# Performance work log

Hardware: AMD Instinct MI355X
Metric: run time of the kernel (lower is better)

## Reference

```python
import jax, jax.numpy as jnp
import numpy as np

BATCH, SEQ, D_IN, D_ST = 16, 8192, 64, 128  # in_features=64, out_features(state)=128


def setup_inputs() -> dict:
    key = jax.random.key(0)
    k0, k1, k2, k3 = jax.random.split(key, 4)
    x = jax.random.normal(k0, (BATCH, SEQ, D_IN), dtype=jnp.float32)
    # State-transition matrix A (HiPPO-initialized in the original). We draw a
    # random dense matrix scaled to spectral radius ~0.9 so the 8192-step
    # recurrence stays numerically stable.
    A = jax.random.normal(k1, (D_ST, D_ST), dtype=jnp.float32) * (0.9 / np.sqrt(D_ST))
    Bw = jax.random.normal(k2, (D_ST, D_IN), dtype=jnp.float32) / np.sqrt(D_IN)
    Bb = jnp.zeros((D_ST,), dtype=jnp.float32)  # bias=True on B
    Cw = jax.random.normal(k3, (D_IN, D_ST), dtype=jnp.float32) / np.sqrt(D_ST)
    return {"x": x, "A": A, "Bw": Bw, "Bb": Bb, "Cw": Cw}


def reference(x, A, Bw, Bb, Cw):
    # Discrete linear SSM: h_t = A h_{t-1} + (B x_t + b),  y_t = C h_t
    # Input projection is batched into one big GEMM (not per-step).
    bx = jnp.einsum('bsi,di->bsd', x, Bw) + Bb          # [B,S,D_ST]
    bx_t = jnp.transpose(bx, (1, 0, 2))                  # [S,B,D_ST]

    def step(h, u):
        h = u + h @ A.T                                  # [B,D_ST]
        return h, h

    h0 = jnp.zeros((x.shape[0], A.shape[0]), dtype=x.dtype)
    _, hs = jax.lax.scan(step, h0, bx_t)                 # hs: [S,B,D_ST]
    # Output projection as one big GEMM after the scan.
    y = jnp.einsum('sbd,od->bso', hs, Cw)                # [B,S,D_IN]
    return y
```

## Files before the change

kernel.cpp:

```cpp
#include <hip/hip_runtime.h>


#define SEQ   8192
#define DIN   64
#define LCH   32
#define NCH   (SEQ / LCH)
#define WFULL 48
#define WTOT  112

typedef _Float16 v8h __attribute__((ext_vector_type(8)));
typedef __fp16   v2h __attribute__((ext_vector_type(2)));
typedef float    v4f __attribute__((ext_vector_type(4)));

#define MFMA(a, b, c) __builtin_amdgcn_mfma_f32_16x16x32_f16((a), (b), (c), 0, 0, 0)
#define PKRTZ __builtin_amdgcn_cvt_pkrtz

__device__ __forceinline__ int rho_inv(int p) {
  int m = p >> 4, q = (p >> 2) & 3, r = p & 3;
  int eh = ((r >> 1) << 1) | (m >> 2);
  int e  = (eh << 1) | (r & 1);
  return 32 * (m & 3) + 8 * q + e;
}

__global__ void prep_kernel(const float* __restrict__ A, const float* __restrict__ Bw,
                            const float* __restrict__ Bb, const float* __restrict__ Cw,
                            _Float16* __restrict__ W, float* __restrict__ Bbs) {
  int idx = blockIdx.x * 256 + threadIdx.x;
  float v; int off_hi, off_lo;
  if (idx < 16384) {
    int p = idx >> 7, j = idx & 127;
    v = A[rho_inv(p) * 128 + j]; off_hi = idx; off_lo = idx + 16384;
  } else if (idx < 24576) {
    int i2 = idx - 16384; int p = i2 >> 6, j = i2 & 63;
    v = Bw[rho_inv(p) * 64 + j]; off_hi = 32768 + i2; off_lo = 40960 + i2;
  } else if (idx < 32768) {
    int i2 = idx - 24576;
    v = Cw[i2]; off_hi = 49152 + i2; off_lo = 57344 + i2;
  } else if (idx < 32896) {
    Bbs[idx - 32768] = Bb[rho_inv(idx - 32768)]; return;
  } else return;
  _Float16 hi = (_Float16)v;
  _Float16 lo = (_Float16)(v - (float)hi);
  W[off_hi] = hi; W[off_lo] = lo;
}

__global__ __launch_bounds__(256, 1) void ssm_kernel(
    const float* __restrict__ x, float* __restrict__ y,
    const _Float16* __restrict__ W, const float* __restrict__ Bbs) {
  const int tid = threadIdx.x;
  const int wv  = tid >> 6;
  const int l   = tid & 63;
  const int n   = l & 15;
  const int q   = l >> 4;
  const int c   = blockIdx.x;
  const int t0  = c * LCH, te = t0 + LCH;
  const int ts  = (t0 > WTOT)  ? (t0 - WTOT)  : 0;
  const int tf  = (t0 > WFULL) ? (t0 - WFULL) : 0;

  const _Float16* Ah = W;
  const _Float16* Al = W + 16384;
  const _Float16* Bh = W + 32768;
  const _Float16* Bl = W + 40960;
  const _Float16* Ch = W + 49152;
  const _Float16* Cl = W + 57344;

  v8h afh[2][4], afl[2][4], bwh[2][2], bwl[2][2], cwh[4], cwl[4];
  v4f bb2[2];
#pragma unroll
  for (int i = 0; i < 2; ++i) {
    int row = 16 * (wv + 4 * i) + n;
#pragma unroll
    for (int kt = 0; kt < 4; ++kt) {
      afh[i][kt] = *(const v8h*)(Ah + row * 128 + 32 * kt + 8 * q);
      afl[i][kt] = *(const v8h*)(Al + row * 128 + 32 * kt + 8 * q);
    }
#pragma unroll
    for (int k2 = 0; k2 < 2; ++k2) {
      bwh[i][k2] = *(const v8h*)(Bh + row * 64 + 32 * k2 + 8 * q);
      bwl[i][k2] = *(const v8h*)(Bl + row * 64 + 32 * k2 + 8 * q);
    }
    bb2[i] = *(const v4f*)(Bbs + 16 * (wv + 4 * i) + 4 * q);
  }
  {
    int row = 16 * wv + n;
#pragma unroll
    for (int kt = 0; kt < 4; ++kt) {
      cwh[kt] = *(const v8h*)(Ch + row * 128 + 32 * kt + 8 * q);
      cwl[kt] = *(const v8h*)(Cl + row * 128 + 32 * kt + 8 * q);
    }
  }

  __shared__ _Float16 hx[2][2][4][512];

  const float* xb = x + (size_t)n * (SEQ * DIN) + 8 * q;
  float* yb = y + (size_t)n * (SEQ * DIN);

  v4f bufA[4], bufB[4];
  auto loadx = [&](v4f(&buf)[4], int t) {
    const float* p = xb + (size_t)t * DIN;
    buf[0] = *(const v4f*)(p);
    buf[1] = *(const v4f*)(p + 4);
    buf[2] = *(const v4f*)(p + 32);
    buf[3] = *(const v4f*)(p + 36);
  };

  v8h hf[4], hlo[4];
#pragma unroll
  for (int kt = 0; kt < 4; ++kt) { hf[kt] = v8h{}; hlo[kt] = v8h{}; }

  v4f uA[2], uB[2];

  auto build_u = [&](const v4f(&b)[4], bool full) {
    union { v2h h2[4]; v8h h8; } H0, H1;
    H0.h2[0] = PKRTZ(b[0][0], b[0][1]); H0.h2[1] = PKRTZ(b[0][2], b[0][3]);
    H0.h2[2] = PKRTZ(b[1][0], b[1][1]); H0.h2[3] = PKRTZ(b[1][2], b[1][3]);
    H1.h2[0] = PKRTZ(b[2][0], b[2][1]); H1.h2[1] = PKRTZ(b[2][2], b[2][3]);
    H1.h2[2] = PKRTZ(b[3][0], b[3][1]); H1.h2[3] = PKRTZ(b[3][2], b[3][3]);
    v8h xh0 = H0.h8, xh1 = H1.h8;
#pragma unroll
    for (int i = 0; i < 2; ++i) {
      v4f a = bb2[i];
      a = MFMA(bwh[i][0], xh0, a);
      a = MFMA(bwh[i][1], xh1, a);
      uA[i] = a;
    }
    if (full) {
      float r[16];
#pragma unroll
      for (int i = 0; i < 8; ++i) r[i]     = b[i >> 2][i & 3]       - (float)H0.h8[i];
#pragma unroll
      for (int i = 0; i < 8; ++i) r[8 + i] = b[2 + (i >> 2)][i & 3] - (float)H1.h8[i];
      union { v2h h2[4]; v8h h8; } L0, L1;
      L0.h2[0] = PKRTZ(r[0], r[1]);   L0.h2[1] = PKRTZ(r[2], r[3]);
      L0.h2[2] = PKRTZ(r[4], r[5]);   L0.h2[3] = PKRTZ(r[6], r[7]);
      L1.h2[0] = PKRTZ(r[8], r[9]);   L1.h2[1] = PKRTZ(r[10], r[11]);
      L1.h2[2] = PKRTZ(r[12], r[13]); L1.h2[3] = PKRTZ(r[14], r[15]);
      v8h xl0 = L0.h8, xl1 = L1.h8;
#pragma unroll
      for (int i = 0; i < 2; ++i) {
        v4f a = {0.f, 0.f, 0.f, 0.f};
        a = MFMA(bwl[i][0], xh0, a);
        a = MFMA(bwl[i][1], xh1, a);
        a = MFMA(bwh[i][0], xl0, a);
        a = MFMA(bwh[i][1], xl1, a);
        uB[i] = a;
      }
    }
  };

  auto emit_y = [&](int t) {
    v4f e1 = {0.f,0.f,0.f,0.f}, e2 = {0.f,0.f,0.f,0.f}, e3 = {0.f,0.f,0.f,0.f};
#pragma unroll
    for (int kt = 0; kt < 4; ++kt) e1 = MFMA(cwh[kt], hf[kt],  e1);
#pragma unroll
    for (int kt = 0; kt < 4; ++kt) e2 = MFMA(cwh[kt], hlo[kt], e2);
#pragma unroll
    for (int kt = 0; kt < 4; ++kt) e3 = MFMA(cwl[kt], hf[kt],  e3);
    v4f r = e1 + e2 + e3;
    *(v4f*)(yb + (size_t)t * DIN + 16 * wv + 4 * q) = r;
  };

  auto xwrite = [&](int pr, const v4f& a0, const v4f& a1, bool full) {
    union { v2h h2[4]; v8h h8; } U;
    U.h2[0] = PKRTZ(a0[0], a0[1]); U.h2[1] = PKRTZ(a1[0], a1[1]);
    U.h2[2] = PKRTZ(a0[2], a0[3]); U.h2[3] = PKRTZ(a1[2], a1[3]);
    *(v8h*)&hx[pr][0][wv][l * 8] = U.h8;
    if (full) {
      float r0 = a0[0] - (float)U.h8[0], r1 = a0[1] - (float)U.h8[1];
      float r2 = a1[0] - (float)U.h8[2], r3 = a1[1] - (float)U.h8[3];
      float r4 = a0[2] - (float)U.h8[4], r5 = a0[3] - (float)U.h8[5];
      float r6 = a1[2] - (float)U.h8[6], r7 = a1[3] - (float)U.h8[7];
      union { v2h h2[4]; v8h h8; } L;
      L.h2[0] = PKRTZ(r0, r1); L.h2[1] = PKRTZ(r2, r3);
      L.h2[2] = PKRTZ(r4, r5); L.h2[3] = PKRTZ(r6, r7);
      *(v8h*)&hx[pr][1][wv][l * 8] = L.h8;
    }
  };

  auto step_full = [&](int t, v4f(&bsrc)[4], v4f(&bld)[4], int pr, bool emit) {
    if (emit) emit_y(t - 1);
    v4f c1[2], c2[2], c3[2];
#pragma unroll
    for (int i = 0; i < 2; ++i) {
      c1[i] = uA[i]; c2[i] = uB[i]; c3[i] = v4f{0.f, 0.f, 0.f, 0.f};
    }
#pragma unroll
    for (int kt = 0; kt < 4; ++kt)
#pragma unroll
      for (int i = 0; i < 2; ++i) {
        c1[i] = MFMA(afh[i][kt], hf[kt],  c1[i]);
        c2[i] = MFMA(afl[i][kt], hf[kt],  c2[i]);
        c3[i] = MFMA(afh[i][kt], hlo[kt], c3[i]);
      }
    build_u(bsrc, true);
    int tn = t + 2; if (tn > SEQ - 1) tn = SEQ - 1;
    loadx(bld, tn);
    v4f a0 = c1[0] + c2[0] + c3[0];
    v4f a1 = c1[1] + c2[1] + c3[1];
    xwrite(pr, a0, a1, true);
    __syncthreads();
#pragma unroll
    for (int kt = 0; kt < 4; ++kt) {
      hf[kt]  = *(const v8h*)&hx[pr][0][kt][l * 8];
      hlo[kt] = *(const v8h*)&hx[pr][1][kt][l * 8];
    }
  };

  auto step_cheap = [&](int t, v4f(&bsrc)[4], v4f(&bld)[4], int pr) {
    v4f c1[2];
#pragma unroll
    for (int i = 0; i < 2; ++i) c1[i] = uA[i];
#pragma unroll
    for (int kt = 0; kt < 4; ++kt)
#pragma unroll
      for (int i = 0; i < 2; ++i) c1[i] = MFMA(afh[i][kt], hf[kt], c1[i]);
    build_u(bsrc, (t + 1) >= tf);
    loadx(bld, t + 2);
    xwrite(pr, c1[0], c1[1], false);
    __syncthreads();
#pragma unroll
    for (int kt = 0; kt < 4; ++kt) hf[kt] = *(const v8h*)&hx[pr][0][kt][l * 8];
  };

  loadx(bufA, ts);
  loadx(bufB, ts + 1);
  build_u(bufA, ts >= tf);

  for (int t = ts; t < tf; t += 2) {
    step_cheap(t,     bufB, bufA, 0);
    step_cheap(t + 1, bufA, bufB, 1);
  }
  for (int t = tf; t < t0; t += 2) {
    step_full(t,     bufB, bufA, 0, false);
    step_full(t + 1, bufA, bufB, 1, false);
  }
  for (int t = t0; t < te; t += 2) {
    step_full(t,     bufB, bufA, 0, t > t0);
    step_full(t + 1, bufA, bufB, 1, true);
  }
  emit_y(te - 1);
}

extern "C" void kernel_launch(void* const* d_in, const int* in_sizes, int n_in,
                              void* d_out, int out_size, void* d_ws, size_t ws_size,
                              hipStream_t stream) {
  const float* x  = (const float*)d_in[0];
  const float* A  = (const float*)d_in[1];
  const float* Bw = (const float*)d_in[2];
  const float* Bb = (const float*)d_in[3];
  const float* Cw = (const float*)d_in[4];
  float* y = (float*)d_out;

  _Float16* W   = (_Float16*)d_ws;
  float*    Bbs = (float*)(W + 65536);

  prep_kernel<<<129, 256, 0, stream>>>(A, Bw, Bb, Cw, W, Bbs);
  ssm_kernel<<<NCH, 256, 0, stream>>>(x, y, W, Bbs);
}
```

Measured before the change: 102.3 us.

## Replace warmup-window recurrence with two-pass chunked scan using precomputed powers of A

Drops the per-chunk 112-step warmup recomputation. A first pass computes each 16-step chunk's local final state, and a second pass combines the previous up to 7 chunk states with precomputed powers of A (A^16 through A^96, built by small matmul kernels) to form each chunk's initial state. It then reruns the chunk to emit y. MFMA accumulation chains are also split into independent partial sums to shorten dependency latency. The cost is nine extra small kernel launches, two passes over x, and a truncated combine that depends on A's spectral decay.

Result: slower. 135.9 us (+32.8%).

```diff
diff --git a/kernel.cpp b/kernel.cpp
--- a/kernel.cpp
+++ b/kernel.cpp
@@ -3,10 +3,9 @@
 
 #define SEQ   8192
 #define DIN   64
-#define LCH   32
+#define LCH   16
 #define NCH   (SEQ / LCH)
-#define WFULL 48
-#define WTOT  112
+#define KCOMB 7
 
 typedef _Float16 v8h __attribute__((ext_vector_type(8)));
 typedef __fp16   v2h __attribute__((ext_vector_type(2)));
@@ -14,39 +13,93 @@
 
 #define MFMA(a, b, c) __builtin_amdgcn_mfma_f32_16x16x32_f16((a), (b), (c), 0, 0, 0)
 #define PKRTZ __builtin_amdgcn_cvt_pkrtz
-
+#define Z4 (v4f{0.f, 0.f, 0.f, 0.f})
+
+
+__device__ __forceinline__ int rho_fwd(int lidx) {
+  int kt = lidx >> 5, q = (lidx >> 3) & 3, e = lidx & 7;
+  int eh = e >> 1;
+  int m = kt + 4 * (eh & 1);
+  int r = 2 * (eh >> 1) + (e & 1);
+  return 16 * m + 4 * q + r;
+}
 __device__ __forceinline__ int rho_inv(int p) {
   int m = p >> 4, q = (p >> 2) & 3, r = p & 3;
   int eh = ((r >> 1) << 1) | (m >> 2);
   int e  = (eh << 1) | (r & 1);
   return 32 * (m & 3) + 8 * q + e;
 }
-
-__global__ void prep_kernel(const float* __restrict__ A, const float* __restrict__ Bw,
-                            const float* __restrict__ Bb, const float* __restrict__ Cw,
-                            _Float16* __restrict__ W, float* __restrict__ Bbs) {
+__device__ __forceinline__ void pack_hl(float v, _Float16* hp, _Float16* lp) {
+  _Float16 h = (_Float16)v;
+  *hp = h; *lp = (_Float16)(v - (float)h);
+}
+
+__global__ void mmk(const float* x0, const float* y0, float* d0,
+                    const float* x1, const float* y1, float* d1,
+                    const float* x2, const float* y2, float* d2) {
+  int which = blockIdx.x >> 6;
+  const float* X = (which == 0) ? x0 : ((which == 1) ? x1 : x2);
+  const float* Y = (which == 0) ? y0 : ((which == 1) ? y1 : y2);
+  float*       D = (which == 0) ? d0 : ((which == 1) ? d1 : d2);
+  int idx = (blockIdx.x & 63) * 256 + threadIdx.x;
+  int i = idx >> 7, j = idx & 127;
+  float s = 0.f;
+  for (int k = 0; k < 128; ++k) s = fmaf(X[i * 128 + k], Y[k * 128 + j], s);
+  D[idx] = s;
+}
+
+__global__ void packk(const float* __restrict__ A, const float* __restrict__ Bw,
+                      const float* __restrict__ Bb, const float* __restrict__ Cw,
+                      const float* __restrict__ pw, _Float16* __restrict__ F,
+                      float* __restrict__ Bbs) {
   int idx = blockIdx.x * 256 + threadIdx.x;
-  float v; int off_hi, off_lo;
   if (idx < 16384) {
-    int p = idx >> 7, j = idx & 127;
-    v = A[rho_inv(p) * 128 + j]; off_hi = idx; off_lo = idx + 16384;
+    int i = idx >> 7, j = idx & 127;
+    int o = rho_fwd(i) * 128 + j;
+    pack_hl(A[idx], F + o, F + 16384 + o);
   } else if (idx < 24576) {
-    int i2 = idx - 16384; int p = i2 >> 6, j = i2 & 63;
-    v = Bw[rho_inv(p) * 64 + j]; off_hi = 32768 + i2; off_lo = 40960 + i2;
+    int p = idx - 16384; int i = p >> 6, j = p & 63;
+    int o = rho_fwd(i) * 64 + j;
+    pack_hl(Bw[p], F + 32768 + o, F + 40960 + o);
   } else if (idx < 32768) {
-    int i2 = idx - 24576;
-    v = Cw[i2]; off_hi = 49152 + i2; off_lo = 57344 + i2;
+    int p = idx - 24576;
+    pack_hl(Cw[p], F + 49152 + p, F + 57344 + p);
   } else if (idx < 32896) {
-    Bbs[idx - 32768] = Bb[rho_inv(idx - 32768)]; return;
-  } else return;
-  _Float16 hi = (_Float16)v;
-  _Float16 lo = (_Float16)(v - (float)hi);
-  W[off_hi] = hi; W[off_lo] = lo;
-}
-
-__global__ __launch_bounds__(256, 1) void ssm_kernel(
-    const float* __restrict__ x, float* __restrict__ y,
-    const _Float16* __restrict__ W, const float* __restrict__ Bbs) {
+    int i = idx - 32768;
+    Bbs[i] = Bb[rho_inv(i)];
+  } else if (idx < 147584) {
+    int p = idx - 32896;
+    int k = p >> 14, r = p & 16383;
+    int i = r >> 7, j = r & 127;
+    float v = (k == 0) ? ((i == j) ? 1.f : 0.f) : pw[(k + 2) * 16384 + r];
+    int o = rho_fwd(i) * 128 + j;
+    pack_hl(v, F + 65536 + k * 16384 + o, F + 180224 + k * 16384 + o);
+  }
+}
+
+__device__ __forceinline__ void split16(const v4f* b, v8h& xh0, v8h& xh1,
+                                        v8h& xl0, v8h& xl1) {
+  union { v2h h2[4]; v8h h8; } H0, H1;
+  H0.h2[0] = PKRTZ(b[0][0], b[0][1]); H0.h2[1] = PKRTZ(b[0][2], b[0][3]);
+  H0.h2[2] = PKRTZ(b[1][0], b[1][1]); H0.h2[3] = PKRTZ(b[1][2], b[1][3]);
+  H1.h2[0] = PKRTZ(b[2][0], b[2][1]); H1.h2[1] = PKRTZ(b[2][2], b[2][3]);
+  H1.h2[2] = PKRTZ(b[3][0], b[3][1]); H1.h2[3] = PKRTZ(b[3][2], b[3][3]);
+  float r[16];
+#pragma unroll
+  for (int i = 0; i < 8; ++i) r[i]     = b[i >> 2][i & 3]       - (float)H0.h8[i];
+#pragma unroll
+  for (int i = 0; i < 8; ++i) r[8 + i] = b[2 + (i >> 2)][i & 3] - (float)H1.h8[i];
+  union { v2h h2[4]; v8h h8; } L0, L1;
+  L0.h2[0] = PKRTZ(r[0], r[1]);   L0.h2[1] = PKRTZ(r[2], r[3]);
+  L0.h2[2] = PKRTZ(r[4], r[5]);   L0.h2[3] = PKRTZ(r[6], r[7]);
+  L1.h2[0] = PKRTZ(r[8], r[9]);   L1.h2[1] = PKRTZ(r[10], r[11]);
+  L1.h2[2] = PKRTZ(r[12], r[13]); L1.h2[3] = PKRTZ(r[14], r[15]);
+  xh0 = H0.h8; xh1 = H1.h8; xl0 = L0.h8; xl1 = L1.h8;
+}
+
+__global__ __launch_bounds__(256, 2) void scan1(
+    const float* __restrict__ x, const _Float16* __restrict__ F,
+    const float* __restrict__ Bbs, _Float16* __restrict__ Vbuf) {
   const int tid = threadIdx.x;
   const int wv  = tid >> 6;
   const int l   = tid & 63;
@@ -54,17 +107,13 @@
   const int q   = l >> 4;
   const int c   = blockIdx.x;
   const int t0  = c * LCH, te = t0 + LCH;
-  const int ts  = (t0 > WTOT)  ? (t0 - WTOT)  : 0;
-  const int tf  = (t0 > WFULL) ? (t0 - WFULL) : 0;
-
-  const _Float16* Ah = W;
-  const _Float16* Al = W + 16384;
-  const _Float16* Bh = W + 32768;
-  const _Float16* Bl = W + 40960;
-  const _Float16* Ch = W + 49152;
-  const _Float16* Cl = W + 57344;
-
-  v8h afh[2][4], afl[2][4], bwh[2][2], bwl[2][2], cwh[4], cwl[4];
+
+  const _Float16* Ah = F;
+  const _Float16* Al = F + 16384;
+  const _Float16* Bh = F + 32768;
+  const _Float16* Bl = F + 40960;
+
+  v8h afh[2][4], afl[2][4], bwh[2][2], bwl[2][2];
   v4f bb2[2];
 #pragma unroll
   for (int i = 0; i < 2; ++i) {
@@ -81,123 +130,255 @@
     }
     bb2[i] = *(const v4f*)(Bbs + 16 * (wv + 4 * i) + 4 * q);
   }
-  {
-    int row = 16 * wv + n;
-#pragma unroll
-    for (int kt = 0; kt < 4; ++kt) {
-      cwh[kt] = *(const v8h*)(Ch + row * 128 + 32 * kt + 8 * q);
-      cwl[kt] = *(const v8h*)(Cl + row * 128 + 32 * kt + 8 * q);
-    }
-  }
 
   __shared__ _Float16 hx[2][2][4][512];
 
   const float* xb = x + (size_t)n * (SEQ * DIN) + 8 * q;
-  float* yb = y + (size_t)n * (SEQ * DIN);
-
-  v4f bufA[4], bufB[4];
+  v4f bufA[4], bufB[4], uA[2], uB[2];
   auto loadx = [&](v4f(&buf)[4], int t) {
     const float* p = xb + (size_t)t * DIN;
-    buf[0] = *(const v4f*)(p);
-    buf[1] = *(const v4f*)(p + 4);
-    buf[2] = *(const v4f*)(p + 32);
-    buf[3] = *(const v4f*)(p + 36);
-  };
-
-  v8h hf[4], hlo[4];
-#pragma unroll
-  for (int kt = 0; kt < 4; ++kt) { hf[kt] = v8h{}; hlo[kt] = v8h{}; }
-
-  v4f uA[2], uB[2];
-
-  auto build_u = [&](const v4f(&b)[4], bool full) {
-    union { v2h h2[4]; v8h h8; } H0, H1;
-    H0.h2[0] = PKRTZ(b[0][0], b[0][1]); H0.h2[1] = PKRTZ(b[0][2], b[0][3]);
-    H0.h2[2] = PKRTZ(b[1][0], b[1][1]); H0.h2[3] = PKRTZ(b[1][2], b[1][3]);
-    H1.h2[0] = PKRTZ(b[2][0], b[2][1]); H1.h2[1] = PKRTZ(b[2][2], b[2][3]);
-    H1.h2[2] = PKRTZ(b[3][0], b[3][1]); H1.h2[3] = PKRTZ(b[3][2], b[3][3]);
-    v8h xh0 = H0.h8, xh1 = H1.h8;
+    buf[0] = *(const v4f*)(p);     buf[1] = *(const v4f*)(p + 4);
+    buf[2] = *(const v4f*)(p + 32); buf[3] = *(const v4f*)(p + 36);
+  };
+  auto build_u = [&](const v4f(&b)[4]) {
+    v8h xh0, xh1, xl0, xl1;
+    split16(b, xh0, xh1, xl0, xl1);
 #pragma unroll
     for (int i = 0; i < 2; ++i) {
       v4f a = bb2[i];
       a = MFMA(bwh[i][0], xh0, a);
       a = MFMA(bwh[i][1], xh1, a);
       uA[i] = a;
-    }
-    if (full) {
-      float r[16];
-#pragma unroll
-      for (int i = 0; i < 8; ++i) r[i]     = b[i >> 2][i & 3]       - (float)H0.h8[i];
-#pragma unroll
-      for (int i = 0; i < 8; ++i) r[8 + i] = b[2 + (i >> 2)][i & 3] - (float)H1.h8[i];
-      union { v2h h2[4]; v8h h8; } L0, L1;
-      L0.h2[0] = PKRTZ(r[0], r[1]);   L0.h2[1] = PKRTZ(r[2], r[3]);
-      L0.h2[2] = PKRTZ(r[4], r[5]);   L0.h2[3] = PKRTZ(r[6], r[7]);
-      L1.h2[0] = PKRTZ(r[8], r[9]);   L1.h2[1] = PKRTZ(r[10], r[11]);
-      L1.h2[2] = PKRTZ(r[12], r[13]); L1.h2[3] = PKRTZ(r[14], r[15]);
-      v8h xl0 = L0.h8, xl1 = L1.h8;
-#pragma unroll
-      for (int i = 0; i < 2; ++i) {
-        v4f a = {0.f, 0.f, 0.f, 0.f};
-        a = MFMA(bwl[i][0], xh0, a);
-        a = MFMA(bwl[i][1], xh1, a);
-        a = MFMA(bwh[i][0], xl0, a);
-        a = MFMA(bwh[i][1], xl1, a);
-        uB[i] = a;
-      }
-    }
-  };
-
-  auto emit_y = [&](int t) {
-    v4f e1 = {0.f,0.f,0.f,0.f}, e2 = {0.f,0.f,0.f,0.f}, e3 = {0.f,0.f,0.f,0.f};
-#pragma unroll
-    for (int kt = 0; kt < 4; ++kt) e1 = MFMA(cwh[kt], hf[kt],  e1);
-#pragma unroll
-    for (int kt = 0; kt < 4; ++kt) e2 = MFMA(cwh[kt], hlo[kt], e2);
-#pragma unroll
-    for (int kt = 0; kt < 4; ++kt) e3 = MFMA(cwl[kt], hf[kt],  e3);
-    v4f r = e1 + e2 + e3;
-    *(v4f*)(yb + (size_t)t * DIN + 16 * wv + 4 * q) = r;
-  };
-
-  auto xwrite = [&](int pr, const v4f& a0, const v4f& a1, bool full) {
+      v4f b1 = MFMA(bwl[i][0], xh0, Z4);
+      b1 = MFMA(bwl[i][1], xh1, b1);
+      v4f b2 = MFMA(bwh[i][0], xl0, Z4);
+      b2 = MFMA(bwh[i][1], xl1, b2);
+      uB[i] = b1 + b2;
+    }
+  };
+  auto xwrite = [&](int pr, const v4f& a0, const v4f& a1) {
     union { v2h h2[4]; v8h h8; } U;
     U.h2[0] = PKRTZ(a0[0], a0[1]); U.h2[1] = PKRTZ(a1[0], a1[1]);
     U.h2[2] = PKRTZ(a0[2], a0[3]); U.h2[3] = PKRTZ(a1[2], a1[3]);
     *(v8h*)&hx[pr][0][wv][l * 8] = U.h8;
-    if (full) {
-      float r0 = a0[0] - (float)U.h8[0], r1 = a0[1] - (float)U.h8[1];
-      float r2 = a1[0] - (float)U.h8[2], r3 = a1[1] - (float)U.h8[3];
-      float r4 = a0[2] - (float)U.h8[4], r5 = a0[3] - (float)U.h8[5];
-      float r6 = a1[2] - (float)U.h8[6], r7 = a1[3] - (float)U.h8[7];
-      union { v2h h2[4]; v8h h8; } L;
-      L.h2[0] = PKRTZ(r0, r1); L.h2[1] = PKRTZ(r2, r3);
-      L.h2[2] = PKRTZ(r4, r5); L.h2[3] = PKRTZ(r6, r7);
-      *(v8h*)&hx[pr][1][wv][l * 8] = L.h8;
-    }
-  };
-
+    float r0 = a0[0] - (float)U.h8[0], r1 = a0[1] - (float)U.h8[1];
+    float r2 = a1[0] - (float)U.h8[2], r3 = a1[1] - (float)U.h8[3];
+    float r4 = a0[2] - (float)U.h8[4], r5 = a0[3] - (float)U.h8[5];
+    float r6 = a1[2] - (float)U.h8[6], r7 = a1[3] - (float)U.h8[7];
+    union { v2h h2[4]; v8h h8; } L;
+    L.h2[0] = PKRTZ(r0, r1); L.h2[1] = PKRTZ(r2, r3);
+    L.h2[2] = PKRTZ(r4, r5); L.h2[3] = PKRTZ(r6, r7);
+    *(v8h*)&hx[pr][1][wv][l * 8] = L.h8;
+  };
+
+  v8h hf[4], hlo[4];
+#pragma unroll
+  for (int kt = 0; kt < 4; ++kt) { hf[kt] = v8h{}; hlo[kt] = v8h{}; }
+
+  auto step_full = [&](int t, v4f(&bsrc)[4], v4f(&bld)[4], int pr) {
+    v4f acc[2];
+#pragma unroll
+    for (int i = 0; i < 2; ++i) {
+      v4f a = MFMA(afh[i][0], hf[0], uA[i]);
+      a     = MFMA(afh[i][1], hf[1], a);
+      v4f b = MFMA(afh[i][2], hf[2], Z4);
+      b     = MFMA(afh[i][3], hf[3], b);
+      v4f c2a = MFMA(afl[i][0], hf[0], uB[i]);
+      c2a     = MFMA(afl[i][1], hf[1], c2a);
+      v4f c2b = MFMA(afl[i][2], hf[2], Z4);
+      c2b     = MFMA(afl[i][3], hf[3], c2b);
+      v4f c3a = MFMA(afh[i][0], hlo[0], Z4);
+      c3a     = MFMA(afh[i][1], hlo[1], c3a);
+      v4f c3b = MFMA(afh[i][2], hlo[2], Z4);
+      c3b     = MFMA(afh[i][3], hlo[3], c3b);
+      acc[i] = (a + b) + (c2a + c2b) + (c3a + c3b);
+    }
+    build_u(bsrc);
+    int tn = t + 2; if (tn > SEQ - 1) tn = SEQ - 1;
+    loadx(bld, tn);
+    xwrite(pr, acc[0], acc[1]);
+    __syncthreads();
+#pragma unroll
+    for (int kt = 0; kt < 4; ++kt) {
+      hf[kt]  = *(const v8h*)&hx[pr][0][kt][l * 8];
+      hlo[kt] = *(const v8h*)&hx[pr][1][kt][l * 8];
+    }
+  };
+
+  loadx(bufA, t0);
+  loadx(bufB, t0 + 1);
+  build_u(bufA);
+  for (int t = t0; t < te; t += 2) {
+    step_full(t,     bufB, bufA, 0);
+    step_full(t + 1, bufA, bufB, 1);
+  }
+  const v8h* sh = (const v8h*)&hx[1][0][0][0];
+  const v8h* sl = (const v8h*)&hx[1][1][0][0];
+  v8h* vb = (v8h*)(Vbuf + (size_t)c * 4096);
+  vb[tid] = sh[tid];
+  vb[256 + tid] = sl[tid];
+}
+
+__global__ __launch_bounds__(256, 2) void scan2(
+    const float* __restrict__ x, float* __restrict__ y,
+    const _Float16* __restrict__ F, const float* __restrict__ Bbs,
+    const _Float16* __restrict__ Vbuf) {
+  const int tid = threadIdx.x;
+  const int wv  = tid >> 6;
+  const int l   = tid & 63;
+  const int n   = l & 15;
+  const int q   = l >> 4;
+  const int c   = blockIdx.x;
+  const int t0  = c * LCH, te = t0 + LCH;
+
+  const _Float16* Ah = F;
+  const _Float16* Al = F + 16384;
+  const _Float16* Bh = F + 32768;
+  const _Float16* Bl = F + 40960;
+  const _Float16* Ch = F + 49152;
+  const _Float16* Cl = F + 57344;
+
+  v8h afh[2][4], afl[2][4], bwh[2][2], bwl[2][2], cwh[4], cwl[4];
+  v4f bb2[2];
+#pragma unroll
+  for (int i = 0; i < 2; ++i) {
+    int row = 16 * (wv + 4 * i) + n;
+#pragma unroll
+    for (int kt = 0; kt < 4; ++kt) {
+      afh[i][kt] = *(const v8h*)(Ah + row * 128 + 32 * kt + 8 * q);
+      afl[i][kt] = *(const v8h*)(Al + row * 128 + 32 * kt + 8 * q);
+    }
+#pragma unroll
+    for (int k2 = 0; k2 < 2; ++k2) {
+      bwh[i][k2] = *(const v8h*)(Bh + row * 64 + 32 * k2 + 8 * q);
+      bwl[i][k2] = *(const v8h*)(Bl + row * 64 + 32 * k2 + 8 * q);
+    }
+    bb2[i] = *(const v4f*)(Bbs + 16 * (wv + 4 * i) + 4 * q);
+  }
+  {
+    int row = 16 * wv + n;
+#pragma unroll
+    for (int kt = 0; kt < 4; ++kt) {
+      cwh[kt] = *(const v8h*)(Ch + row * 128 + 32 * kt + 8 * q);
+      cwl[kt] = *(const v8h*)(Cl + row * 128 + 32 * kt + 8 * q);
+    }
+  }
+
+  __shared__ _Float16 hx[2][2][4][512];
+
+  v8h hf[4], hlo[4];
+#pragma unroll
+  for (int kt = 0; kt < 4; ++kt) { hf[kt] = v8h{}; hlo[kt] = v8h{}; }
+
+  auto xwrite = [&](int pr, const v4f& a0, const v4f& a1) {
+    union { v2h h2[4]; v8h h8; } U;
+    U.h2[0] = PKRTZ(a0[0], a0[1]); U.h2[1] = PKRTZ(a1[0], a1[1]);
+    U.h2[2] = PKRTZ(a0[2], a0[3]); U.h2[3] = PKRTZ(a1[2], a1[3]);
+    *(v8h*)&hx[pr][0][wv][l * 8] = U.h8;
+    float r0 = a0[0] - (float)U.h8[0], r1 = a0[1] - (float)U.h8[1];
+    float r2 = a1[0] - (float)U.h8[2], r3 = a1[1] - (float)U.h8[3];
+    float r4 = a0[2] - (float)U.h8[4], r5 = a0[3] - (float)U.h8[5];
+    float r6 = a1[2] - (float)U.h8[6], r7 = a1[3] - (float)U.h8[7];
+    union { v2h h2[4]; v8h h8; } L;
+    L.h2[0] = PKRTZ(r0, r1); L.h2[1] = PKRTZ(r2, r3);
+    L.h2[2] = PKRTZ(r4, r5); L.h2[3] = PKRTZ(r6, r7);
+    *(v8h*)&hx[pr][1][wv][l * 8] = L.h8;
+  };
+
+  if (c > 0) {
+    const int kmax = (c < KCOMB) ? c : KCOMB;
+    v4f c1[2] = {Z4, Z4}, c2[2] = {Z4, Z4}, c3[2] = {Z4, Z4};
+    for (int k = 1; k <= kmax; ++k) {
+      const v8h* vb = (const v8h*)(Vbuf + (size_t)(c - k) * 4096);
+      v8h vh[4], vl[4];
+#pragma unroll
+      for (int kt = 0; kt < 4; ++kt) {
+        vh[kt] = vb[kt * 64 + l];
+        vl[kt] = vb[256 + kt * 64 + l];
+      }
+      const _Float16* th = F + 65536  + (k - 1) * 16384;
+      const _Float16* tl = F + 180224 + (k - 1) * 16384;
+#pragma unroll
+      for (int i = 0; i < 2; ++i) {
+        int row = 16 * (wv + 4 * i) + n;
+#pragma unroll
+        for (int kt = 0; kt < 4; ++kt) {
+          v8h tfh = *(const v8h*)(th + row * 128 + 32 * kt + 8 * q);
+          v8h tfl = *(const v8h*)(tl + row * 128 + 32 * kt + 8 * q);
+          c1[i] = MFMA(tfh, vh[kt], c1[i]);
+          c2[i] = MFMA(tfl, vh[kt], c2[i]);
+          c3[i] = MFMA(tfh, vl[kt], c3[i]);
+        }
+      }
+    }
+    v4f a0 = c1[0] + c2[0] + c3[0];
+    v4f a1 = c1[1] + c2[1] + c3[1];
+    xwrite(1, a0, a1);
+    __syncthreads();
+#pragma unroll
+    for (int kt = 0; kt < 4; ++kt) {
+      hf[kt]  = *(const v8h*)&hx[1][0][kt][l * 8];
+      hlo[kt] = *(const v8h*)&hx[1][1][kt][l * 8];
+    }
+  }
+
+  const float* xb = x + (size_t)n * (SEQ * DIN) + 8 * q;
+  float* yb = y + (size_t)n * (SEQ * DIN);
+  v4f bufA[4], bufB[4], uA[2], uB[2];
+  auto loadx = [&](v4f(&buf)[4], int t) {
+    const float* p = xb + (size_t)t * DIN;
+    buf[0] = *(const v4f*)(p);      buf[1] = *(const v4f*)(p + 4);
+    buf[2] = *(const v4f*)(p + 32); buf[3] = *(const v4f*)(p + 36);
+  };
+  auto build_u = [&](const v4f(&b)[4]) {
+    v8h xh0, xh1, xl0, xl1;
+    split16(b, xh0, xh1, xl0, xl1);
+#pragma unroll
+    for (int i = 0; i < 2; ++i) {
+      v4f a = bb2[i];
+      a = MFMA(bwh[i][0], xh0, a);
+      a = MFMA(bwh[i][1], xh1, a);
+      uA[i] = a;
+      v4f b1 = MFMA(bwl[i][0], xh0, Z4);
+      b1 = MFMA(bwl[i][1], xh1, b1);
+      v4f b2 = MFMA(bwh[i][0], xl0, Z4);
+      b2 = MFMA(bwh[i][1], xl1, b2);
+      uB[i] = b1 + b2;
+    }
+  };
+  auto emit_y = [&](int t) {
+    v4f e1a = MFMA(cwh[1], hf[1], MFMA(cwh[0], hf[0], Z4));
+    v4f e1b = MFMA(cwh[3], hf[3], MFMA(cwh[2], hf[2], Z4));
+    v4f e2a = MFMA(cwh[1], hlo[1], MFMA(cwh[0], hlo[0], Z4));
+    v4f e2b = MFMA(cwh[3], hlo[3], MFMA(cwh[2], hlo[2], Z4));
+    v4f e3a = MFMA(cwl[1], hf[1], MFMA(cwl[0], hf[0], Z4));
+    v4f e3b = MFMA(cwl[3], hf[3], MFMA(cwl[2], hf[2], Z4));
+    v4f r = (e1a + e1b) + (e2a + e2b) + (e3a + e3b);
+    *(v4f*)(yb + (size_t)t * DIN + 16 * wv + 4 * q) = r;
+  };
   auto step_full = [&](int t, v4f(&bsrc)[4], v4f(&bld)[4], int pr, bool emit) {
     if (emit) emit_y(t - 1);
-    v4f c1[2], c2[2], c3[2];
+    v4f acc[2];
 #pragma unroll
     for (int i = 0; i < 2; ++i) {
-      c1[i] = uA[i]; c2[i] = uB[i]; c3[i] = v4f{0.f, 0.f, 0.f, 0.f};
-    }
-#pragma unroll
-    for (int kt = 0; kt < 4; ++kt)
-#pragma unroll
-      for (int i = 0; i < 2; ++i) {
-        c1[i] = MFMA(afh[i][kt], hf[kt],  c1[i]);
-        c2[i] = MFMA(afl[i][kt], hf[kt],  c2[i]);
-        c3[i] = MFMA(afh[i][kt], hlo[kt], c3[i]);
-      }
-    build_u(bsrc, true);
+      v4f a = MFMA(afh[i][0], hf[0], uA[i]);
+      a     = MFMA(afh[i][1], hf[1], a);
+      v4f b = MFMA(afh[i][2], hf[2], Z4);
+      b     = MFMA(afh[i][3], hf[3], b);
+      v4f c2a = MFMA(afl[i][0], hf[0], uB[i]);
+      c2a     = MFMA(afl[i][1], hf[1], c2a);
+      v4f c2b = MFMA(afl[i][2], hf[2], Z4);
+      c2b     = MFMA(afl[i][3], hf[3], c2b);
+      v4f c3a = MFMA(afh[i][0], hlo[0], Z4);
+      c3a     = MFMA(afh[i][1], hlo[1], c3a);
+      v4f c3b = MFMA(afh[i][2], hlo[2], Z4);
+      c3b     = MFMA(afh[i][3], hlo[3], c3b);
+      acc[i] = (a + b) + (c2a + c2b) + (c3a + c3b);
+    }
+    build_u(bsrc);
     int tn = t + 2; if (tn > SEQ - 1) tn = SEQ - 1;
     loadx(bld, tn);
-    v4f a0 = c1[0] + c2[0] + c3[0];
-    v4f a1 = c1[1] + c2[1] + c3[1];
-    xwrite(pr, a0, a1, true);
+    xwrite(pr, acc[0], acc[1]);
     __syncthreads();
 #pragma unroll
     for (int kt = 0; kt < 4; ++kt) {
@@ -206,34 +387,9 @@
     }
   };
 
-  auto step_cheap = [&](int t, v4f(&bsrc)[4], v4f(&bld)[4], int pr) {
-    v4f c1[2];
-#pragma unroll
-    for (int i = 0; i < 2; ++i) c1[i] = uA[i];
-#pragma unroll
-    for (int kt = 0; kt < 4; ++kt)
-#pragma unroll
-      for (int i = 0; i < 2; ++i) c1[i] = MFMA(afh[i][kt], hf[kt], c1[i]);
-    build_u(bsrc, (t + 1) >= tf);
-    loadx(bld, t + 2);
-    xwrite(pr, c1[0], c1[1], false);
-    __syncthreads();
-#pragma unroll
-    for (int kt = 0; kt < 4; ++kt) hf[kt] = *(const v8h*)&hx[pr][0][kt][l * 8];
-  };
-
-  loadx(bufA, ts);
-  loadx(bufB, ts + 1);
-  build_u(bufA, ts >= tf);
-
-  for (int t = ts; t < tf; t += 2) {
-    step_cheap(t,     bufB, bufA, 0);
-    step_cheap(t + 1, bufA, bufB, 1);
-  }
-  for (int t = tf; t < t0; t += 2) {
-    step_full(t,     bufB, bufA, 0, false);
-    step_full(t + 1, bufA, bufB, 1, false);
-  }
+  loadx(bufA, t0);
+  loadx(bufB, t0 + 1);
+  build_u(bufA);
   for (int t = t0; t < te; t += 2) {
     step_full(t,     bufB, bufA, 0, t > t0);
     step_full(t + 1, bufA, bufB, 1, true);
@@ -251,9 +407,29 @@
   const float* Cw = (const float*)d_in[4];
   float* y = (float*)d_out;
 
-  _Float16* W   = (_Float16*)d_ws;
-  float*    Bbs = (float*)(W + 65536);
-
-  prep_kernel<<<129, 256, 0, stream>>>(A, Bw, Bb, Cw, W, Bbs);
-  ssm_kernel<<<NCH, 256, 0, stream>>>(x, y, W, Bbs);
-}
+  _Float16* F    = (_Float16*)d_ws;
+  float*    Bbs  = (float*)((char*)d_ws + 589824);
+  float*    pw   = (float*)((char*)d_ws + 590336);
+  _Float16* Vbuf = (_Float16*)((char*)d_ws + 1180160);
+
+  float* A2  = pw;
+  float* A4  = pw + 1 * 16384;
+  float* A8  = pw + 2 * 16384;
+  float* A16 = pw + 3 * 16384;
+  float* A32 = pw + 4 * 16384;
+  float* A48 = pw + 5 * 16384;
+  float* A64 = pw + 6 * 16384;
+  float* A80 = pw + 7 * 16384;
+  float* A96 = pw + 8 * 16384;
+
+  mmk<<<64,  256, 0, stream>>>(A,   A,   A2,  nullptr, nullptr, nullptr, nullptr, nullptr, nullptr);
+  mmk<<<64,  256, 0, stream>>>(A2,  A2,  A4,  nullptr, nullptr, nullptr, nullptr, nullptr, nullptr);
+  mmk<<<64,  256, 0, stream>>>(A4,  A4,  A8,  nullptr, nullptr, nullptr, nullptr, nullptr, nullptr);
+  mmk<<<64,  256, 0, stream>>>(A8,  A8,  A16, nullptr, nullptr, nullptr, nullptr, nullptr, nullptr);
+  mmk<<<64,  256, 0, stream>>>(A16, A16, A32, nullptr, nullptr, nullptr, nullptr, nullptr, nullptr);
+  mmk<<<128, 256, 0, stream>>>(A32, A16, A48, A32, A32, A64, nullptr, nullptr, nullptr);
+  mmk<<<128, 256, 0, stream>>>(A64, A16, A80, A64, A32, A96, nullptr, nullptr, nullptr);
+  packk<<<577, 256, 0, stream>>>(A, Bw, Bb, Cw, pw, F, Bbs);
+  scan1<<<NCH, 256, 0, stream>>>(x, F, Bbs, Vbuf);
+  scan2<<<NCH, 256, 0, stream>>>(x, y, F, Bbs, Vbuf);
+}
```
